# Kernel tuning notes

Hardware: AMD Instinct MI355X
Metric: run time of the kernel (lower is better)

Reference implementation:

```python
import jax, jax.numpy as jnp
import numpy as np

NUM = 256
T = 0.05
MAXITER = 5


def _constants():
    P = jnp.eye(NUM, dtype=jnp.float32)                  # [num, num]
    Pd = jnp.diff(P, axis=0) / T                          # [num-1, num]
    Pdd = jnp.diff(Pd, axis=0) / T                        # [num-2, num]
    A_eq = P[0:1]                                         # [1, num]
    A_control = jnp.vstack([P, -P, Pd, -Pd, Pdd, -Pdd])   # [6*num-6, num]
    # rho = rho_projection = 1, A_projection = I
    cost = jnp.eye(NUM, dtype=jnp.float32) + A_control.T @ A_control
    cost_mat = jnp.vstack([
        jnp.hstack([cost, A_eq.T]),
        jnp.hstack([A_eq, jnp.zeros((1, 1), dtype=jnp.float32)]),
    ])                                                    # [num+1, num+1]
    return A_eq, A_control, cost_mat


def setup_inputs() -> dict:
    key = jax.random.key(0)
    ks = jax.random.split(key, 8)
    B, IND, H = 4096, 260, 1024
    NC = 6 * NUM - 6
    OUT = NUM + NC
    return {
        "inp": jax.random.normal(ks[0], (B, IND), jnp.float32),
        "steer_init": 0.1 * jax.random.normal(ks[1], (B, 1), jnp.float32),
        "steer_samples": 0.5 * jax.random.normal(ks[2], (B, NUM), jnp.float32),
        "steer_max": jnp.float32(1.0),
        "steer_min": jnp.float32(-1.0),
        "steerdot_max": jnp.float32(2.0),
        "steerdot_min": jnp.float32(-2.0),
        "steerddot_max": jnp.float32(4.0),
        "steerddot_min": jnp.float32(-4.0),
        "median_": jnp.zeros((IND,), jnp.float32),
        "iqr_": jnp.ones((IND,), jnp.float32),
        "W1": 0.02 * jax.random.normal(ks[3], (IND, H), jnp.float32),
        "b1": jnp.zeros((H,), jnp.float32),
        "W2": 0.02 * jax.random.normal(ks[4], (H, OUT), jnp.float32),
        "b2": jnp.zeros((OUT,), jnp.float32),
    }


def reference(inp, steer_init, steer_samples, steer_max, steer_min,
              steerdot_max, steerdot_min, steerddot_max, steerddot_min,
              median_, iqr_, W1, b1, W2, b2):
    A_eq, A_control, cost_mat = _constants()
    B = inp.shape[0]
    NC = A_control.shape[0]
    n1, n2 = NUM - 1, NUM - 2

    # Note: original computes (inp-median)/iqr then overwrites with inp.
    inp_norm = inp
    h = jax.nn.relu(inp_norm @ W1 + b1)
    neural_out = h @ W2 + b2                              # [B, num + nc]
    lamda = neural_out[:, :NUM]
    s = jnp.maximum(0.0, neural_out[:, NUM:NUM + NC])

    b_eq = steer_init * jnp.ones((B, 1), jnp.float32)     # [B, 1]
    ones_n = jnp.ones((B, NUM), jnp.float32)
    ones_n1 = jnp.ones((B, n1), jnp.float32)
    ones_n2 = jnp.ones((B, n2), jnp.float32)
    b_control = jnp.hstack([
        steer_max * ones_n, -steer_min * ones_n,
        steerdot_max * ones_n1, -steerdot_min * ones_n1,
        steerddot_max * ones_n2, -steerddot_min * ones_n2,
    ])                                                    # [B, nc]

    def step(carry, _):
        lamda, s = carry
        b_aug = b_control - s
        # rho = rho_projection = 1, A_projection = I
        lincost = -lamda - steer_samples - b_aug @ A_control   # [B, num]
        rhs = jnp.hstack([-lincost, b_eq])                     # [B, num+1]
        sol = jnp.linalg.solve(cost_mat, rhs.T).T
        steer_proj = sol[:, :NUM]
        As = steer_proj @ A_control.T                          # [B, nc]
        s_new = jnp.maximum(0.0, -As + b_control)
        res_vec = As - b_control + s_new
        res_norm = jnp.linalg.norm(res_vec, axis=1)
        lamda_new = lamda - res_vec @ A_control
        fp = (jnp.linalg.norm(s - s_new, axis=1)
              + jnp.linalg.norm(lamda - lamda_new, axis=1))
        return (lamda_new, s_new), (steer_proj, res_norm, fp)

    (_, _), (projs, prim_stack, fp_stack) = jax.lax.scan(
        step, (lamda, s), None, length=MAXITER)
    steer_projected = projs[-1]
    acc_primal = jnp.sum(prim_stack, axis=0) / MAXITER
    acc_fixed = jnp.sum(fp_stack, axis=0) / MAXITER
    return steer_projected, prim_stack, fp_stack, acc_primal, acc_fixed
```

## Files before the change

kernel.cpp:

```cpp
#include <hip/hip_runtime.h>
#include <cstddef>


#define NUMV 256
#define QP_ITERS 5
#define NO_LD 1792
#define LSCALE 2048.0f
#define INV_LSCALE (1.0f / 2048.0f)

typedef _Float16 f16x4 __attribute__((ext_vector_type(4)));
typedef _Float16 f16x8 __attribute__((ext_vector_type(8)));
typedef float f32x4 __attribute__((ext_vector_type(4)));

struct FacT {
  double invd[256];
  double l1[257];
  double l2[258];
  double z[256];
  float  zcf[256];
};

constexpr double csqrt_(double x) {
  double g = (x > 1.0) ? x : 1.0;
  for (int i = 0; i < 64; ++i) g = 0.5 * (g + x / g);
  return g;
}

constexpr FacT make_fac() {
  FacT f{};
  const double T = 0.05, a = 1.0 / (T * T), b2 = a * a;
  double c0[256] = {}, c1[255] = {}, c2[254] = {};
  double dd[256] = {}, l1[256] = {}, l2[256] = {};
  for (int j = 0; j < 256; j++) {
    double cd1 = (j == 0 || j == 255) ? 1.0 : 2.0;
    double cd2 = (j == 0 || j == 255) ? 1.0 : ((j == 1 || j == 254) ? 5.0 : 6.0);
    c0[j] = 3.0 + 2.0 * a * cd1 + 2.0 * b2 * cd2;
  }
  for (int j = 0; j < 255; j++) c1[j] = -2.0 * a + 2.0 * b2 * ((j == 0 || j == 254) ? -2.0 : -4.0);
  for (int j = 0; j < 254; j++) c2[j] = 2.0 * b2;
  dd[0] = csqrt_(c0[0]); l1[0] = 0.0; l2[0] = 0.0;
  l1[1] = c1[0] / dd[0]; l2[1] = 0.0;
  dd[1] = csqrt_(c0[1] - l1[1] * l1[1]);
  for (int j = 2; j < 256; j++) {
    l2[j] = c2[j - 2] / dd[j - 2];
    l1[j] = (c1[j - 1] - l2[j] * l1[j - 1]) / dd[j - 1];
    dd[j] = csqrt_(c0[j] - l1[j] * l1[j] - l2[j] * l2[j]);
  }
  for (int j = 0; j < 256; j++) f.invd[j] = 1.0 / dd[j];
  for (int j = 0; j < 256; j++) f.l1[j] = l1[j];
  f.l1[256] = 0.0;
  for (int j = 0; j < 256; j++) f.l2[j] = l2[j];
  f.l2[256] = 0.0; f.l2[257] = 0.0;
  double w[256] = {}, zz[256] = {};
  w[0] = 1.0 / dd[0];
  w[1] = (-l1[1] * w[0]) / dd[1];
  for (int j = 2; j < 256; j++) w[j] = (-l1[j] * w[j - 1] - l2[j] * w[j - 2]) / dd[j];
  zz[255] = w[255] / dd[255];
  zz[254] = (w[254] - l1[255] * zz[255]) / dd[254];
  for (int j = 253; j >= 0; j--)
    zz[j] = (w[j] - l1[j + 1] * zz[j + 1] - l2[j + 2] * zz[j + 2]) / dd[j];
  for (int j = 0; j < 256; j++) f.z[j] = zz[j];
  for (int j = 0; j < 256; j++) f.zcf[j] = (float)(zz[j] / zz[0]);
  return f;
}

constexpr FacT FAC_HOST = make_fac();
__constant__ FacT FAC = FAC_HOST;

struct UQ { float u[64][256]; };

constexpr UQ make_uq(int cbase) {
  UQ q{};
  const double T = 0.05, a = 1.0 / (T * T), b2 = a * a;
  double c0a[256] = {}, c1a[255] = {}, c2a[254] = {};
  double dd[256] = {}, l1[256] = {}, l2[256] = {};
  for (int j = 0; j < 256; j++) {
    double cd1 = (j == 0 || j == 255) ? 1.0 : 2.0;
    double cd2 = (j == 0 || j == 255) ? 1.0 : ((j == 1 || j == 254) ? 5.0 : 6.0);
    c0a[j] = 3.0 + 2.0 * a * cd1 + 2.0 * b2 * cd2;
  }
  for (int j = 0; j < 255; j++) c1a[j] = -2.0 * a + 2.0 * b2 * ((j == 0 || j == 254) ? -2.0 : -4.0);
  for (int j = 0; j < 254; j++) c2a[j] = 2.0 * b2;
  dd[0] = csqrt_(c0a[0]); l1[0] = 0.0; l2[0] = 0.0;
  l1[1] = c1a[0] / dd[0]; l2[1] = 0.0;
  dd[1] = csqrt_(c0a[1] - l1[1] * l1[1]);
  for (int j = 2; j < 256; j++) {
    l2[j] = c2a[j - 2] / dd[j - 2];
    l1[j] = (c1a[j - 1] - l2[j] * l1[j - 1]) / dd[j - 1];
    dd[j] = csqrt_(c0a[j] - l1[j] * l1[j] - l2[j] * l2[j]);
  }
  for (int c = cbase; c < cbase + 64; ++c) {
    double w1 = 0.0, w2 = 0.0;
    for (int j = c; j < 256; ++j) {
      const double rhs = (j == c) ? 1.0 : 0.0;
      const double wj = (rhs - l1[j] * w1 - l2[j] * w2) / dd[j];
      q.u[c - cbase][j] = (float)wj;
      w2 = w1; w1 = wj;
    }
  }
  return q;
}

constexpr UQ UQ0_H = make_uq(0);
constexpr UQ UQ1_H = make_uq(64);
constexpr UQ UQ2_H = make_uq(128);
constexpr UQ UQ3_H = make_uq(192);
__constant__ UQ UFQ0 = UQ0_H;
__constant__ UQ UFQ1 = UQ1_H;
__constant__ UQ UFQ2 = UQ2_H;
__constant__ UQ UFQ3 = UQ3_H;

__global__ __launch_bounds__(256) void split_u(
    _Float16* __restrict__ Uh, _Float16* __restrict__ Ul, float* __restrict__ zc)
{
  const int c = blockIdx.x, j = threadIdx.x;
  float wf;
  if (c < 64)       wf = UFQ0.u[c][j];
  else if (c < 128) wf = UFQ1.u[c - 64][j];
  else if (c < 192) wf = UFQ2.u[c - 128][j];
  else              wf = UFQ3.u[c - 192][j];
  const _Float16 h = (_Float16)wf;
  Uh[(size_t)c * 256 + j] = h;
  Ul[(size_t)c * 256 + j] = (_Float16)((wf - (float)h) * LSCALE);
  if (c == 0) zc[j] = FAC.zcf[j];
}

__global__ __launch_bounds__(64) void gemm_g(
    const _Float16* __restrict__ Uh, const _Float16* __restrict__ Ul,
    _Float16* __restrict__ Gh, _Float16* __restrict__ Gl)
{
  const int lane = threadIdx.x;
  const int lr = lane & 15, lg = lane >> 4;
  const int m0 = blockIdx.x * 16, n0 = blockIdx.y * 32;
  f32x4 accH[2], accL[2];
#pragma unroll
  for (int nf = 0; nf < 2; nf++) { accH[nf] = (f32x4)0.0f; accL[nf] = (f32x4)0.0f; }
  const size_t arow = (size_t)(m0 + lr) * 256 + lg * 8;
#pragma unroll 2
  for (int k0 = 0; k0 < 256; k0 += 32) {
    const f16x8 ah = *reinterpret_cast<const f16x8*>(&Uh[arow + k0]);
    const f16x8 al = *reinterpret_cast<const f16x8*>(&Ul[arow + k0]);
#pragma unroll
    for (int nf = 0; nf < 2; nf++) {
      const size_t bidx = (size_t)(n0 + nf * 16 + lr) * 256 + k0 + lg * 8;
      const f16x8 bh = *reinterpret_cast<const f16x8*>(&Uh[bidx]);
      const f16x8 bl = *reinterpret_cast<const f16x8*>(&Ul[bidx]);
      accH[nf] = __builtin_amdgcn_mfma_f32_16x16x32_f16(ah, bh, accH[nf], 0, 0, 0);
      accL[nf] = __builtin_amdgcn_mfma_f32_16x16x32_f16(ah, bl, accL[nf], 0, 0, 0);
      accL[nf] = __builtin_amdgcn_mfma_f32_16x16x32_f16(al, bh, accL[nf], 0, 0, 0);
    }
  }
  const int row0 = m0 + lg * 4;
#pragma unroll
  for (int nf = 0; nf < 2; nf++) {
    const int col = n0 + nf * 16 + lr;
    const double zcd = FAC.z[col] / FAC.z[0];
#pragma unroll
    for (int r = 0; r < 4; r++) {
      const int row = row0 + r;
      const float g = accH[nf][r] + accL[nf][r] * INV_LSCALE
                    - (float)(FAC.z[row] * zcd);
      const _Float16 gh = (_Float16)g;
      Gh[(size_t)row * 256 + col] = gh;
      Gl[(size_t)row * 256 + col] = (_Float16)((g - (float)gh) * LSCALE);
    }
  }
}

__global__ __launch_bounds__(256) void transpose_cvt(
    const float* __restrict__ in, _Float16* __restrict__ out, int K, int N)
{
  __shared__ float t[32][33];
  const int bk = blockIdx.x * 32, bn = blockIdx.y * 32;
  const int x = threadIdx.x, y = threadIdx.y;
  for (int yy = y; yy < 32; yy += 8) {
    const int k = bk + yy, n = bn + x;
    t[yy][x] = (k < K && n < N) ? in[(size_t)k * N + n] : 0.f;
  }
  __syncthreads();
  for (int yy = y; yy < 32; yy += 8) {
    const int n = bn + yy, k = bk + x;
    if (n < N && k < K) out[(size_t)n * K + k] = (_Float16)t[x][yy];
  }
}

template<bool A_FP32, bool OUT_H16>
__global__ __launch_bounds__(256) void mfma_gemm(
    const void* __restrict__ Av, const _Float16* __restrict__ Bt,
    const float* __restrict__ bias, void* __restrict__ Cv,
    int M, int Nv, int K, int lda, int ldk, int ldc)
{
  __shared__ _Float16 At[128][40];
  __shared__ _Float16 Bs[128][40];
  const int tid = threadIdx.x;
  const int lane = tid & 63, wid = tid >> 6;
  const int wr = wid >> 1, wc = wid & 1;
  const int lrow = lane & 15, lb = lane >> 4;
  const int m0 = blockIdx.x * 128, n0 = blockIdx.y * 128;
  const int srow = tid >> 1, skh = (tid & 1) * 16;

  f32x4 acc[4][4];
#pragma unroll
  for (int i = 0; i < 4; i++)
#pragma unroll
    for (int j = 0; j < 4; j++) acc[i][j] = (f32x4)0.0f;

  const int nsteps = (K + 31) / 32;
  for (int t = 0; t < nsteps; ++t) {
    const int k0 = t * 32;
    if (A_FP32) {
      const float* A = (const float*)Av;
#pragma unroll
      for (int i = 0; i < 4; i++) {
        const int k = k0 + skh + i * 4;
        f16x4 hv = {};
        if (k + 4 <= K) {
          const float4 v = *reinterpret_cast<const float4*>(&A[(size_t)(m0 + srow) * lda + k]);
          hv[0] = (_Float16)v.x; hv[1] = (_Float16)v.y;
          hv[2] = (_Float16)v.z; hv[3] = (_Float16)v.w;
        } else if (k < K) {
          for (int e = 0; e < 4; e++)
            if (k + e < K) hv[e] = (_Float16)A[(size_t)(m0 + srow) * lda + k + e];
        }
        *reinterpret_cast<f16x4*>(&At[srow][skh + i * 4]) = hv;
      }
    } else {
      const _Float16* A = (const _Float16*)Av;
#pragma unroll
      for (int i = 0; i < 4; i++) {
        const int k = k0 + skh + i * 4;
        f16x4 hv = {};
        if (k + 4 <= K) hv = *reinterpret_cast<const f16x4*>(&A[(size_t)(m0 + srow) * lda + k]);
        *reinterpret_cast<f16x4*>(&At[srow][skh + i * 4]) = hv;
      }
    }
    {
      const int n = n0 + srow;
#pragma unroll
      for (int i = 0; i < 4; i++) {
        const int k = k0 + skh + i * 4;
        f16x4 hv = {};
        if (n < Nv && k + 4 <= K)
          hv = *reinterpret_cast<const f16x4*>(&Bt[(size_t)n * ldk + k]);
        *reinterpret_cast<f16x4*>(&Bs[srow][skh + i * 4]) = hv;
      }
    }
    __syncthreads();
    f16x8 af[4], bf[4];
#pragma unroll
    for (int i = 0; i < 4; i++)
      af[i] = *reinterpret_cast<const f16x8*>(&At[wr * 64 + i * 16 + lrow][lb * 8]);
#pragma unroll
    for (int j = 0; j < 4; j++)
      bf[j] = *reinterpret_cast<const f16x8*>(&Bs[wc * 64 + j * 16 + lrow][lb * 8]);
#pragma unroll
    for (int i = 0; i < 4; i++)
#pragma unroll
      for (int j = 0; j < 4; j++)
        acc[i][j] = __builtin_amdgcn_mfma_f32_16x16x32_f16(af[i], bf[j], acc[i][j], 0, 0, 0);
    __syncthreads();
  }
#pragma unroll
  for (int i = 0; i < 4; i++) {
#pragma unroll
    for (int j = 0; j < 4; j++) {
      const int gcol = n0 + wc * 64 + j * 16 + lrow;
      if (gcol < Nv) {
        const float bv = bias[gcol];
#pragma unroll
        for (int r = 0; r < 4; r++) {
          const int grow = m0 + wr * 64 + i * 16 + lb * 4 + r;
          float v = acc[i][j][r] + bv;
          if (OUT_H16) {
            v = fmaxf(v, 0.f);
            ((_Float16*)Cv)[(size_t)grow * ldc + gcol] = (_Float16)v;
          } else {
            ((float*)Cv)[(size_t)grow * ldc + gcol] = v;
          }
        }
      }
    }
  }
}

__global__ __launch_bounds__(256) void mfma_gemm64(
    const _Float16* __restrict__ A, const _Float16* __restrict__ Bt,
    const float* __restrict__ bias, float* __restrict__ C,
    int M, int Nv, int K, int lda, int ldk, int ldc)
{
  __shared__ _Float16 At[128][64];
  __shared__ _Float16 Bs[128][64];
  const int tid = threadIdx.x;
  const int lane = tid & 63, wid = tid >> 6;
  const int wr = wid >> 1, wc = wid & 1;
  const int lrow = lane & 15, lb = lane >> 4;
  const int m0 = blockIdx.x * 128, n0 = blockIdx.y * 128;

  const int srow8 = lane >> 3;
  const int kswz = 8 * ((lane & 7) ^ srow8);

  f32x4 acc[4][4];
#pragma unroll
  for (int i = 0; i < 4; i++)
#pragma unroll
    for (int j = 0; j < 4; j++) acc[i][j] = (f32x4)0.0f;

  const int nsteps = K >> 6;
  for (int t = 0; t < nsteps; ++t) {
    const int k0 = t * 64;
#pragma unroll
    for (int c = 0; c < 4; ++c) {
      const int ci = wid * 4 + c;
      const int row = ci * 8 + srow8;
      const _Float16* asrc = &A[(size_t)(m0 + row) * lda + k0 + kswz];
      const _Float16* bsrc = &Bt[(size_t)(n0 + row) * ldk + k0 + kswz];
      __builtin_amdgcn_global_load_lds(
          (const __attribute__((address_space(1))) void*)asrc,
          (__attribute__((address_space(3))) void*)(&At[ci * 8][0]), 16, 0, 0);
      __builtin_amdgcn_global_load_lds(
          (const __attribute__((address_space(1))) void*)bsrc,
          (__attribute__((address_space(3))) void*)(&Bs[ci * 8][0]), 16, 0, 0);
    }
    __syncthreads();
#pragma unroll
    for (int h = 0; h < 2; h++) {
      f16x8 af[4], bf[4];
#pragma unroll
      for (int i = 0; i < 4; i++) {
        const int r = wr * 64 + i * 16 + lrow;
        af[i] = *reinterpret_cast<const f16x8*>(
            &At[r][(h * 32 + lb * 8) ^ ((r & 7) << 3)]);
      }
#pragma unroll
      for (int j = 0; j < 4; j++) {
        const int r = wc * 64 + j * 16 + lrow;
        bf[j] = *reinterpret_cast<const f16x8*>(
            &Bs[r][(h * 32 + lb * 8) ^ ((r & 7) << 3)]);
      }
#pragma unroll
      for (int i = 0; i < 4; i++)
#pragma unroll
        for (int j = 0; j < 4; j++)
          acc[i][j] = __builtin_amdgcn_mfma_f32_16x16x32_f16(af[i], bf[j], acc[i][j], 0, 0, 0);
    }
    __syncthreads();
  }
#pragma unroll
  for (int i = 0; i < 4; i++) {
#pragma unroll
    for (int j = 0; j < 4; j++) {
      const int gcol = n0 + wc * 64 + j * 16 + lrow;
      if (gcol < Nv) {
        const float bv = bias[gcol];
#pragma unroll
        for (int r = 0; r < 4; r++) {
          const int grow = m0 + wr * 64 + i * 16 + lb * 4 + r;
          C[(size_t)grow * ldc + gcol] = acc[i][j][r] + bv;
        }
      }
    }
  }
}

__global__ __launch_bounds__(1024) void qp_solve5(
    const _Float16* __restrict__ Gh, const _Float16* __restrict__ Gl,
    const float* __restrict__ beq, const float* __restrict__ zc,
    const float* __restrict__ NO, const float* __restrict__ ss,
    const float* __restrict__ p_smax, const float* __restrict__ p_smin,
    const float* __restrict__ p_sdmax, const float* __restrict__ p_sdmin,
    const float* __restrict__ p_sddmax, const float* __restrict__ p_sddmin,
    float* __restrict__ out, int B)
{
  __shared__ float xsA[16][264], xsB[16][264];
  __shared__ _Float16 vhs[16][264], vls[16][264];
  __shared__ float zcs[256], beqs[16];
  __shared__ float red[16][4][3];
  const int tid = threadIdx.x;
  const int wave = tid >> 6, lane = tid & 63;
  const int lr = lane & 15, lg = lane >> 4;
  const int m0 = blockIdx.x * 16;
  const int n0 = wave * 16;
  const int j = tid & 255, half = tid >> 8;

  const float smax = *p_smax, smin = *p_smin;
  const float sdmax = *p_sdmax, sdmin = *p_sdmin;
  const float sddmax = *p_sddmax, sddmin = *p_sddmin;
  const float K0 = smax + smin, K1 = sdmax + sdmin, K2 = sddmax + sddmin;
  const float invT = 20.f, invT2 = 400.f;
  const bool h1 = j < 255, h2 = j < 254;

  f16x8 gh_r[8];
#pragma unroll
  for (int kk = 0; kk < 8; kk++) {
    const size_t bidx = (size_t)(n0 + lr) * 256 + kk * 32 + lg * 8;
    gh_r[kk] = *reinterpret_cast<const f16x8*>(&Gh[bidx]);
  }

  float lamr[4], ssv[4];
#pragma unroll
  for (int rr = 0; rr < 4; rr++) {
    const int rl = half * 4 + rr;
    const int gr = m0 + rl;
    const float* no = NO + (size_t)gr * NO_LD;
    ssv[rr] = ss[(size_t)gr * NUMV + j];
    lamr[rr] = no[j];
    const float D0 = K0 - fmaxf(0.f, no[256 + j]) + fmaxf(0.f, no[512 + j]);
    const float D1j = h1 ? (K1 - fmaxf(0.f, no[768 + j]) + fmaxf(0.f, no[1023 + j])) : 0.f;
    const float D1m = (j >= 1) ? (K1 - fmaxf(0.f, no[768 + j - 1]) + fmaxf(0.f, no[1023 + j - 1])) : 0.f;
    const float D2j = h2 ? (K2 - fmaxf(0.f, no[1278 + j]) + fmaxf(0.f, no[1532 + j])) : 0.f;
    const float D2m1 = (j >= 1 && h1) ? (K2 - fmaxf(0.f, no[1278 + j - 1]) + fmaxf(0.f, no[1532 + j - 1])) : 0.f;
    const float D2m2 = (j >= 2) ? (K2 - fmaxf(0.f, no[1278 + j - 2]) + fmaxf(0.f, no[1532 + j - 2])) : 0.f;
    const float vn = lamr[rr] + ssv[rr]
                   + D0 + (D1m - D1j) * invT + (D2m2 - 2.f * D2m1 + D2j) * invT2;
    const _Float16 vh16 = (_Float16)vn;
    vhs[rl][j] = vh16;
    vls[rl][j] = (_Float16)((vn - (float)vh16) * LSCALE);
  }
  if (tid < 256) zcs[tid] = zc[tid];
  if (tid < 16) {
    beqs[tid] = beq[m0 + tid];
    xsA[tid][0] = 0.f; xsA[tid][1] = 0.f; xsA[tid][258] = 0.f; xsA[tid][259] = 0.f;
    xsB[tid][0] = 0.f; xsB[tid][1] = 0.f; xsB[tid][258] = 0.f; xsB[tid][259] = 0.f;
  }
  float accP = 0.f, accF = 0.f;

  const size_t primOff = (size_t)B * NUMV;
  const size_t fpOff = primOff + (size_t)QP_ITERS * B;
  const size_t accPOff = fpOff + (size_t)QP_ITERS * B;
  const size_t accFOff = accPOff + (size_t)B;

  float (*xc)[264] = xsA;
  float (*xp)[264] = xsB;

  __syncthreads();

  for (int it = 0; it < QP_ITERS; ++it) {
    f32x4 accH = (f32x4)0.0f, accL = (f32x4)0.0f;
#pragma unroll
    for (int kk = 0; kk < 8; kk++) {
      const f16x8 ah = *reinterpret_cast<const f16x8*>(&vhs[lr][kk * 32 + lg * 8]);
      const f16x8 al = *reinterpret_cast<const f16x8*>(&vls[lr][kk * 32 + lg * 8]);
      const f16x8 bl = *reinterpret_cast<const f16x8*>(
          &Gl[(size_t)(n0 + lr) * 256 + kk * 32 + lg * 8]);
      accH = __builtin_amdgcn_mfma_f32_16x16x32_f16(ah, gh_r[kk], accH, 0, 0, 0);
      accL = __builtin_amdgcn_mfma_f32_16x16x32_f16(ah, bl, accL, 0, 0, 0);
      accL = __builtin_amdgcn_mfma_f32_16x16x32_f16(al, gh_r[kk], accL, 0, 0, 0);
    }
    {
      const int r0l = lg * 4;
      const int col = n0 + lr;
      const float zv = zcs[col];
#pragma unroll
      for (int r = 0; r < 4; r++)
        xc[r0l + r][col + 2] = accH[r] + accL[r] * INV_LSCALE + beqs[r0l + r] * zv;
    }
    __syncthreads();

#pragma unroll
    for (int rr = 0; rr < 4; rr++) {
      const int rl = half * 4 + rr;
      const int gr = m0 + rl;
      const float xm2 = xc[rl][j];
      const float xm1 = xc[rl][j + 1];
      const float x0  = xc[rl][j + 2];
      const float x1  = xc[rl][j + 3];
      const float x2  = xc[rl][j + 4];

      const float vj = (x1 - x0) * invT;
      const float aj = (x2 - 2.f * x1 + x0) * invT2;
      const float vm1 = (x0 - xm1) * invT;
      const float am1 = (x1 - 2.f * x0 + xm1) * invT2;
      const float am2 = (x0 - 2.f * xm1 + xm2) * invT2;

      const float rv0a = fmaxf(0.f, x0 - smax), rv0b = fmaxf(0.f, smin - x0);
      const float E0 = rv0a - rv0b;
      float rv1a = 0.f, rv1b = 0.f, rv2a = 0.f, rv2b = 0.f, E1 = 0.f, E2 = 0.f;
      if (h1) { rv1a = fmaxf(0.f, vj - sdmax); rv1b = fmaxf(0.f, sdmin - vj); E1 = rv1a - rv1b; }
      if (h2) { rv2a = fmaxf(0.f, aj - sddmax); rv2b = fmaxf(0.f, sddmin - aj); E2 = rv2a - rv2b; }
      float res2 = rv0a * rv0a + rv0b * rv0b + rv1a * rv1a + rv1b * rv1b
                 + rv2a * rv2a + rv2b * rv2b;

      const float E1m = (j >= 1) ? (fmaxf(0.f, vm1 - sdmax) - fmaxf(0.f, sdmin - vm1)) : 0.f;
      const float E2m1 = (j >= 1 && h1) ? (fmaxf(0.f, am1 - sddmax) - fmaxf(0.f, sddmin - am1)) : 0.f;
      const float E2m2 = (j >= 2) ? (fmaxf(0.f, am2 - sddmax) - fmaxf(0.f, sddmin - am2)) : 0.f;

      const float dl = E0 + (E1m - E1) * invT + (E2m2 - 2.f * E2m1 + E2) * invT2;
      const float lnew = lamr[rr] - dl;
      const float fpl2 = dl * dl;
      lamr[rr] = lnew;

      const float sn0a = fmaxf(0.f, smax - x0), sn0b = fmaxf(0.f, x0 - smin);
      float sn1a = 0.f, sn1b = 0.f, sn2a = 0.f, sn2b = 0.f;
      if (h1) { sn1a = fmaxf(0.f, sdmax - vj); sn1b = fmaxf(0.f, vj - sdmin); }
      if (h2) { sn2a = fmaxf(0.f, sddmax - aj); sn2b = fmaxf(0.f, aj - sddmin); }

      float sp0a, sp0b, sp1a = 0.f, sp1b = 0.f, sp2a = 0.f, sp2b = 0.f;
      if (it == 0) {
        const float* no = NO + (size_t)gr * NO_LD;
        sp0a = fmaxf(0.f, no[256 + j]); sp0b = fmaxf(0.f, no[512 + j]);
        if (h1) { sp1a = fmaxf(0.f, no[768 + j]); sp1b = fmaxf(0.f, no[1023 + j]); }
        if (h2) { sp2a = fmaxf(0.f, no[1278 + j]); sp2b = fmaxf(0.f, no[1532 + j]); }
      } else {
        const float p0 = xp[rl][j + 2], p1 = xp[rl][j + 3], p2 = xp[rl][j + 4];
        const float vp = (p1 - p0) * invT;
        const float ap = (p2 - 2.f * p1 + p0) * invT2;
        sp0a = fmaxf(0.f, smax - p0); sp0b = fmaxf(0.f, p0 - smin);
        if (h1) { sp1a = fmaxf(0.f, sdmax - vp); sp1b = fmaxf(0.f, vp - sdmin); }
        if (h2) { sp2a = fmaxf(0.f, sddmax - ap); sp2b = fmaxf(0.f, ap - sddmin); }
      }
      const float d0a = sp0a - sn0a, d0b = sp0b - sn0b;
      const float d1a = sp1a - sn1a, d1b = sp1b - sn1b;
      const float d2a = sp2a - sn2a, d2b = sp2b - sn2b;
      float fps2 = d0a * d0a + d0b * d0b + d1a * d1a + d1b * d1b
                 + d2a * d2a + d2b * d2b;

      const float D0 = fminf(smax, x0) + fmaxf(smin, x0);
      const float D1 = h1 ? (fminf(sdmax, vj) + fmaxf(sdmin, vj)) : 0.f;
      const float D2 = h2 ? (fminf(sddmax, aj) + fmaxf(sddmin, aj)) : 0.f;
      const float D1m = (j >= 1) ? (fminf(sdmax, vm1) + fmaxf(sdmin, vm1)) : 0.f;
      const float D2m1 = (j >= 1 && h1) ? (fminf(sddmax, am1) + fmaxf(sddmin, am1)) : 0.f;
      const float D2m2 = (j >= 2) ? (fminf(sddmax, am2) + fmaxf(sddmin, am2)) : 0.f;

      if (it < QP_ITERS - 1) {
        const float vn = lnew + ssv[rr]
                       + D0 + (D1m - D1) * invT + (D2m2 - 2.f * D2m1 + D2) * invT2;
        const _Float16 vh16 = (_Float16)vn;
        vhs[rl][j] = vh16;
        vls[rl][j] = (_Float16)((vn - (float)vh16) * LSCALE);
      } else {
        out[(size_t)gr * NUMV + j] = x0;
      }

      float a = res2, b = fps2, c = fpl2;
      for (int o = 32; o > 0; o >>= 1) {
        a += __shfl_down(a, o);
        b += __shfl_down(b, o);
        c += __shfl_down(c, o);
      }
      if (lane == 0) { red[wave][rr][0] = a; red[wave][rr][1] = b; red[wave][rr][2] = c; }
    }
    __syncthreads();

    if (tid < 16) {
      const int rl = tid, hf = rl >> 2, rr = rl & 3;
      const int w0 = hf * 4;
      const float r2 = red[w0][rr][0] + red[w0 + 1][rr][0] + red[w0 + 2][rr][0] + red[w0 + 3][rr][0];
      const float s2 = red[w0][rr][1] + red[w0 + 1][rr][1] + red[w0 + 2][rr][1] + red[w0 + 3][rr][1];
      const float l2 = red[w0][rr][2] + red[w0 + 1][rr][2] + red[w0 + 2][rr][2] + red[w0 + 3][rr][2];
      const float pr = sqrtf(r2);
      const float fp = sqrtf(s2) + sqrtf(l2);
      out[primOff + (size_t)it * B + m0 + rl] = pr;
      out[fpOff + (size_t)it * B + m0 + rl] = fp;
      accP += pr; accF += fp;
    }
    float (*t)[264] = xc; xc = xp; xp = t;
  }
  if (tid < 16) {
    out[accPOff + m0 + tid] = accP * (1.f / QP_ITERS);
    out[accFOff + m0 + tid] = accF * (1.f / QP_ITERS);
  }
}

extern "C" void kernel_launch(void* const* d_in, const int* in_sizes, int n_in,
                              void* d_out, int out_size, void* d_ws, size_t ws_size,
                              hipStream_t stream)
{
  const float* inp = (const float*)d_in[0];
  const float* sinit = (const float*)d_in[1];
  const float* ssamp = (const float*)d_in[2];
  const float* p_smax = (const float*)d_in[3];
  const float* p_smin = (const float*)d_in[4];
  const float* p_sdmax = (const float*)d_in[5];
  const float* p_sdmin = (const float*)d_in[6];
  const float* p_sddmax = (const float*)d_in[7];
  const float* p_sddmin = (const float*)d_in[8];
  const float* W1 = (const float*)d_in[11];
  const float* b1 = (const float*)d_in[12];
  const float* W2 = (const float*)d_in[13];
  const float* b2 = (const float*)d_in[14];
  float* out = (float*)d_out;

  const int B = in_sizes[1];
  const int IND = in_sizes[9];
  const int H = in_sizes[12];
  const int OUTN = in_sizes[14];

  char* ws = (char*)d_ws;
  float* NO = (float*)ws;
  char* p = ws + (size_t)B * NO_LD * 4;
  _Float16* hH = (_Float16*)p;
  char* q = p + (size_t)B * H * 2;
  _Float16* W2T = (_Float16*)q;
  char* q2 = q + (size_t)OUTN * H * 2;
  _Float16* W1T = (_Float16*)q2;
  char* r4 = ws + 46137344;
  _Float16* Gh = (_Float16*)r4;
  _Float16* Gl = (_Float16*)(r4 + 131072);
  float* zc = (float*)(r4 + 262144);
  _Float16* Uh = (_Float16*)(r4 + 263168);
  _Float16* Ul = (_Float16*)(r4 + 263168 + 131072);

  split_u<<<256, 256, 0, stream>>>(Uh, Ul, zc);
  {
    dim3 g(16, 8);
    gemm_g<<<g, 64, 0, stream>>>(Uh, Ul, Gh, Gl);
  }
  {
    dim3 g((IND + 31) / 32, (H + 31) / 32), blk(32, 8);
    transpose_cvt<<<g, blk, 0, stream>>>(W1, W1T, IND, H);
  }
  {
    dim3 g((H + 31) / 32, (OUTN + 31) / 32), blk(32, 8);
    transpose_cvt<<<g, blk, 0, stream>>>(W2, W2T, H, OUTN);
  }
  {
    dim3 g(B / 128, H / 128);
    mfma_gemm<true, true><<<g, 256, 0, stream>>>(inp, W1T, b1, hH, B, H, IND, IND, IND, H);
  }
  {
    dim3 g(B / 128, (OUTN + 127) / 128);
    mfma_gemm64<<<g, 256, 0, stream>>>(hH, W2T, b2, NO, B, OUTN, H, H, H, NO_LD);
  }
  qp_solve5<<<B / 16, 1024, 0, stream>>>(Gh, Gl, sinit, zc, NO, ssamp,
                                         p_smax, p_smin, p_sdmax, p_sdmin,
                                         p_sddmax, p_sddmin, out, B);
}
```

Measured before the change: 142.7 us.

## Fuse U split into gemm_g and load W1T tiles via direct global-to-LDS

Removes the split_u kernel: gemm_g now reads the constant-memory U rows directly, splits them into high/low fp16 in registers, and writes zc from its first block. The first MLP GEMM's B tile is now loaded with global_load_lds into a 32-wide XOR-swizzled LDS layout instead of register-staged stores. To support this, W1T is padded to a K stride of 288 with zeros. This saves a launch and a register round trip, but it relies on the padding and the swizzle being correct and drops the bounds checks on B loads.

```diff
diff --git a/kernel.cpp b/kernel.cpp
--- a/kernel.cpp
+++ b/kernel.cpp
@@ -110,41 +110,46 @@
 __constant__ UQ UFQ2 = UQ2_H;
 __constant__ UQ UFQ3 = UQ3_H;
 
-__global__ __launch_bounds__(256) void split_u(
-    _Float16* __restrict__ Uh, _Float16* __restrict__ Ul, float* __restrict__ zc)
-{
-  const int c = blockIdx.x, j = threadIdx.x;
-  float wf;
-  if (c < 64)       wf = UFQ0.u[c][j];
-  else if (c < 128) wf = UFQ1.u[c - 64][j];
-  else if (c < 192) wf = UFQ2.u[c - 128][j];
-  else              wf = UFQ3.u[c - 192][j];
-  const _Float16 h = (_Float16)wf;
-  Uh[(size_t)c * 256 + j] = h;
-  Ul[(size_t)c * 256 + j] = (_Float16)((wf - (float)h) * LSCALE);
-  if (c == 0) zc[j] = FAC.zcf[j];
+__device__ __forceinline__ const float* uq_row(int c) {
+  if (c < 64)  return UFQ0.u[c];
+  if (c < 128) return UFQ1.u[c - 64];
+  if (c < 192) return UFQ2.u[c - 128];
+  return UFQ3.u[c - 192];
+}
+
+__device__ __forceinline__ void split8(const float* __restrict__ w, f16x8& h, f16x8& l) {
+#pragma unroll
+  for (int e = 0; e < 8; e++) {
+    const float x = w[e];
+    const _Float16 hh = (_Float16)x;
+    h[e] = hh;
+    l[e] = (_Float16)((x - (float)hh) * LSCALE);
+  }
 }
 
 __global__ __launch_bounds__(64) void gemm_g(
-    const _Float16* __restrict__ Uh, const _Float16* __restrict__ Ul,
-    _Float16* __restrict__ Gh, _Float16* __restrict__ Gl)
+    _Float16* __restrict__ Gh, _Float16* __restrict__ Gl, float* __restrict__ zc)
 {
   const int lane = threadIdx.x;
   const int lr = lane & 15, lg = lane >> 4;
   const int m0 = blockIdx.x * 16, n0 = blockIdx.y * 32;
+  if (blockIdx.x == 0 && blockIdx.y == 0) {
+    for (int t = lane; t < 256; t += 64) zc[t] = FAC.zcf[t];
+  }
   f32x4 accH[2], accL[2];
 #pragma unroll
   for (int nf = 0; nf < 2; nf++) { accH[nf] = (f32x4)0.0f; accL[nf] = (f32x4)0.0f; }
-  const size_t arow = (size_t)(m0 + lr) * 256 + lg * 8;
+  const float* arow = uq_row(m0 + lr);
+  const float* brow0 = uq_row(n0 + lr);
+  const float* brow1 = uq_row(n0 + 16 + lr);
 #pragma unroll 2
   for (int k0 = 0; k0 < 256; k0 += 32) {
-    const f16x8 ah = *reinterpret_cast<const f16x8*>(&Uh[arow + k0]);
-    const f16x8 al = *reinterpret_cast<const f16x8*>(&Ul[arow + k0]);
+    f16x8 ah, al;
+    split8(arow + k0 + lg * 8, ah, al);
 #pragma unroll
     for (int nf = 0; nf < 2; nf++) {
-      const size_t bidx = (size_t)(n0 + nf * 16 + lr) * 256 + k0 + lg * 8;
-      const f16x8 bh = *reinterpret_cast<const f16x8*>(&Uh[bidx]);
-      const f16x8 bl = *reinterpret_cast<const f16x8*>(&Ul[bidx]);
+      f16x8 bh, bl;
+      split8((nf ? brow1 : brow0) + k0 + lg * 8, bh, bl);
       accH[nf] = __builtin_amdgcn_mfma_f32_16x16x32_f16(ah, bh, accH[nf], 0, 0, 0);
       accL[nf] = __builtin_amdgcn_mfma_f32_16x16x32_f16(ah, bl, accL[nf], 0, 0, 0);
       accL[nf] = __builtin_amdgcn_mfma_f32_16x16x32_f16(al, bh, accL[nf], 0, 0, 0);
@@ -168,7 +173,7 @@
 }
 
 __global__ __launch_bounds__(256) void transpose_cvt(
-    const float* __restrict__ in, _Float16* __restrict__ out, int K, int N)
+    const float* __restrict__ in, _Float16* __restrict__ out, int K, int N, int KP)
 {
   __shared__ float t[32][33];
   const int bk = blockIdx.x * 32, bn = blockIdx.y * 32;
@@ -180,7 +185,7 @@
   __syncthreads();
   for (int yy = y; yy < 32; yy += 8) {
     const int n = bn + yy, k = bk + x;
-    if (n < N && k < K) out[(size_t)n * K + k] = (_Float16)t[x][yy];
+    if (n < N && k < KP) out[(size_t)n * KP + k] = (_Float16)t[x][yy];
   }
 }
 
@@ -191,13 +196,16 @@
     int M, int Nv, int K, int lda, int ldk, int ldc)
 {
   __shared__ _Float16 At[128][40];
-  __shared__ _Float16 Bs[128][40];
+  __shared__ _Float16 Bs[128][32];
   const int tid = threadIdx.x;
   const int lane = tid & 63, wid = tid >> 6;
   const int wr = wid >> 1, wc = wid & 1;
   const int lrow = lane & 15, lb = lane >> 4;
   const int m0 = blockIdx.x * 128, n0 = blockIdx.y * 128;
   const int srow = tid >> 1, skh = (tid & 1) * 16;
+
+  const int rl4 = lane >> 2;
+  const int kswz = 8 * ((lane & 3) ^ (rl4 & 3));
 
   f32x4 acc[4][4];
 #pragma unroll
@@ -235,14 +243,13 @@
       }
     }
     {
-      const int n = n0 + srow;
-#pragma unroll
-      for (int i = 0; i < 4; i++) {
-        const int k = k0 + skh + i * 4;
-        f16x4 hv = {};
-        if (n < Nv && k + 4 <= K)
-          hv = *reinterpret_cast<const f16x4*>(&Bt[(size_t)n * ldk + k]);
-        *reinterpret_cast<f16x4*>(&Bs[srow][skh + i * 4]) = hv;
+#pragma unroll
+      for (int c = 0; c < 2; ++c) {
+        const int ci = wid * 2 + c;
+        const _Float16* bsrc = &Bt[(size_t)(n0 + ci * 16 + rl4) * ldk + k0 + kswz];
+        __builtin_amdgcn_global_load_lds(
+            (const __attribute__((address_space(1))) void*)bsrc,
+            (__attribute__((address_space(3))) void*)(&Bs[ci * 16][0]), 16, 0, 0);
       }
     }
     __syncthreads();
@@ -251,8 +258,10 @@
     for (int i = 0; i < 4; i++)
       af[i] = *reinterpret_cast<const f16x8*>(&At[wr * 64 + i * 16 + lrow][lb * 8]);
 #pragma unroll
-    for (int j = 0; j < 4; j++)
-      bf[j] = *reinterpret_cast<const f16x8*>(&Bs[wc * 64 + j * 16 + lrow][lb * 8]);
+    for (int j = 0; j < 4; j++) {
+      const int r = wc * 64 + j * 16 + lrow;
+      bf[j] = *reinterpret_cast<const f16x8*>(&Bs[r][(lb * 8) ^ ((r & 3) << 3)]);
+    }
 #pragma unroll
     for (int i = 0; i < 4; i++)
 #pragma unroll
@@ -584,6 +593,7 @@
   const int IND = in_sizes[9];
   const int H = in_sizes[12];
   const int OUTN = in_sizes[14];
+  const int KP1 = 288;
 
   char* ws = (char*)d_ws;
   float* NO = (float*)ws;
@@ -597,25 +607,22 @@
   _Float16* Gh = (_Float16*)r4;
   _Float16* Gl = (_Float16*)(r4 + 131072);
   float* zc = (float*)(r4 + 262144);
-  _Float16* Uh = (_Float16*)(r4 + 263168);
-  _Float16* Ul = (_Float16*)(r4 + 263168 + 131072);
-
-  split_u<<<256, 256, 0, stream>>>(Uh, Ul, zc);
+
   {
     dim3 g(16, 8);
-    gemm_g<<<g, 64, 0, stream>>>(Uh, Ul, Gh, Gl);
+    gemm_g<<<g, 64, 0, stream>>>(Gh, Gl, zc);
   }
   {
-    dim3 g((IND + 31) / 32, (H + 31) / 32), blk(32, 8);
-    transpose_cvt<<<g, blk, 0, stream>>>(W1, W1T, IND, H);
+    dim3 g((KP1 + 31) / 32, (H + 31) / 32), blk(32, 8);
+    transpose_cvt<<<g, blk, 0, stream>>>(W1, W1T, IND, H, KP1);
   }
   {
     dim3 g((H + 31) / 32, (OUTN + 31) / 32), blk(32, 8);
-    transpose_cvt<<<g, blk, 0, stream>>>(W2, W2T, H, OUTN);
+    transpose_cvt<<<g, blk, 0, stream>>>(W2, W2T, H, OUTN, H);
   }
   {
     dim3 g(B / 128, H / 128);
-    mfma_gemm<true, true><<<g, 256, 0, stream>>>(inp, W1T, b1, hH, B, H, IND, IND, IND, H);
+    mfma_gemm<true, true><<<g, 256, 0, stream>>>(inp, W1T, b1, hH, B, H, IND, IND, KP1, H);
   }
   {
     dim3 g(B / 128, (OUTN + 127) / 128);
```

Measured after the change: 135.4 us. 1.05x faster.
